# Kernel optimization log

Measured on AMD Instinct MI355X. Metric: run time of the kernel, lower is better.

Reference implementation:

```python
import jax, jax.numpy as jnp
import numpy as np

INPUT_SIZE = 256
HIDDEN_SIZE = 512
BATCH = 128
SEQ_LEN = 512


def setup_inputs() -> dict:
    key = jax.random.key(0)
    ks = jax.random.split(key, 7)
    I, H = INPUT_SIZE, HIDDEN_SIZE
    s_i = 1.0 / np.sqrt(I)
    s_h = 1.0 / np.sqrt(H)
    return {
        "x": jax.random.normal(ks[0], (BATCH, SEQ_LEN, I), dtype=jnp.float32),
        "delta_t": jax.random.uniform(ks[1], (BATCH, SEQ_LEN, 1), dtype=jnp.float32) * 10.0,
        "W": jax.random.normal(ks[2], (I, 4 * H), dtype=jnp.float32) * s_i,
        "U": jax.random.normal(ks[3], (H, 4 * H), dtype=jnp.float32) * s_h,
        "b": jnp.zeros((4 * H,), dtype=jnp.float32),
        "W_d": jax.random.normal(ks[4], (H, H), dtype=jnp.float32) * s_h,
        "b_d": jnp.zeros((H,), dtype=jnp.float32),
    }


def reference(x, delta_t, W, U, b, W_d, b_d):
    # T-LSTM (Baytas et al. 2017): time-decay cell decomposition + standard LSTM gates.
    B, S, _ = x.shape
    H = W_d.shape[0]
    h0 = jnp.zeros((B, H), dtype=x.dtype)
    c0 = jnp.zeros((B, H), dtype=x.dtype)
    E = jnp.float32(np.e)

    def step(carry, inp):
        h, c = carry
        x_t, dt = inp  # (B, I), (B, 1)
        # subspace decomposition with elapsed-time decay g(dt) = 1/log(e + dt)
        c_s = jnp.tanh(c @ W_d + b_d)          # short-term memory
        g = 1.0 / jnp.log(E + dt)              # (B, 1) decay, broadcast over H
        c_adj = c - c_s + c_s * g              # adjusted previous cell state
        z = x_t @ W + h @ U + b                # fused gate pre-activations (B, 4H)
        i_g, f_g, o_g, c_tilde = jnp.split(z, 4, axis=-1)
        i_g = jax.nn.sigmoid(i_g)
        f_g = jax.nn.sigmoid(f_g)
        o_g = jax.nn.sigmoid(o_g)
        c_tilde = jnp.tanh(c_tilde)
        c_new = f_g * c_adj + i_g * c_tilde
        h_new = o_g * jnp.tanh(c_new)
        return (h_new, c_new), h_new

    xs = (jnp.swapaxes(x, 0, 1), jnp.swapaxes(delta_t, 0, 1))  # time-major
    (h_t, c_t), hs = jax.lax.scan(step, (h0, c0), xs)
    outputs = jnp.swapaxes(hs, 0, 1)  # (B, S, H)
    return outputs, h_t, c_t
```

## Files before the change

### kernel.cpp

```cpp
#include <hip/hip_runtime.h>

typedef unsigned short u16;
typedef unsigned int u32;
typedef unsigned long long u64;
typedef __attribute__((ext_vector_type(8))) short short8;
typedef __attribute__((ext_vector_type(4))) float f32x4;

constexpr int BATCH = 128, SEQ = 512, ISZ = 256, HSZ = 512, G4H = 2048;
constexpr int KZ   = ISZ + HSZ;
constexpr int NGRP = 8,  MR  = BATCH / NGRP;
constexpr int NCW  = 32, CPW = HSZ / NCW;
constexpr int LDBZ = KZ + 8, LDBC = HSZ + 8, LDH = HSZ + 8;
constexpr int BH   = BATCH * HSZ;
constexpr size_t BSH = (size_t)BATCH * SEQ * HSZ;

constexpr size_t WUT_OFF = 0;
constexpr size_t WDT_OFF = WUT_OFF + (size_t)G4H * KZ * 2;
constexpr size_t HBF_OFF = WDT_OFF + (size_t)HSZ * HSZ * 2;
constexpr size_t CBF_OFF = HBF_OFF + (size_t)2 * BH * 2;
constexpr size_t FLG_OFF = CBF_OFF + (size_t)2 * BH * 2;

constexpr int BZ_OFF  = 0;
constexpr int BC_OFF  = BZ_OFF  + 64 * LDBZ * 2;
constexpr int HS_OFF  = BC_OFF  + 16 * LDBC * 2;
constexpr int ZS_OFF  = HS_OFF  + MR * LDH * 2;
constexpr int CFL_OFF = ZS_OFF  + 5 * 256 * 4;
constexpr int BL_OFF  = CFL_OFF + MR * CPW * 4;
constexpr int LDS_BYTES = BL_OFF + 5 * CPW * 4;

__device__ __forceinline__ u16 f2bf(float f) {
  unsigned u = __float_as_uint(f);
  u += 0x7fffu + ((u >> 16) & 1u);
  return (u16)(u >> 16);
}

__device__ __forceinline__ u32 cvtpk(float lo, float hi) {
  u32 r;
  asm("v_cvt_pk_bf16_f32 %0, %1, %2" : "=v"(r) : "v"(lo), "v"(hi));
  return r;
}

__device__ __forceinline__ short8 cvt_bf8(float4 a, float4 b) {
  union { u32 u[4]; short8 s; } v;
  v.u[0] = cvtpk(a.x, a.y);
  v.u[1] = cvtpk(a.z, a.w);
  v.u[2] = cvtpk(b.x, b.y);
  v.u[3] = cvtpk(b.z, b.w);
  return v.s;
}

__device__ __forceinline__ u64 ld_at64(const void* p) {
  return __hip_atomic_load((const u64*)p, __ATOMIC_RELAXED,
                           __HIP_MEMORY_SCOPE_AGENT);
}
__device__ __forceinline__ void st_at64(void* p, u64 v) {
  __hip_atomic_store((u64*)p, v, __ATOMIC_RELAXED, __HIP_MEMORY_SCOPE_AGENT);
}
__device__ __forceinline__ void st_at32(void* p, u32 v) {
  __hip_atomic_store((u32*)p, v, __ATOMIC_RELAXED, __HIP_MEMORY_SCOPE_AGENT);
}
__device__ __forceinline__ short8 ld_bf8_at(const u16* p) {
  union { u64 u[2]; short8 s; } v;
  v.u[0] = ld_at64(p);
  v.u[1] = ld_at64(p + 4);
  return v.s;
}

__device__ __forceinline__ float sig_f(float x)  { return 1.f / (1.f + __expf(-x)); }
__device__ __forceinline__ float tanh_f(float x) { return 1.f - 2.f / (1.f + __expf(2.f * x)); }

constexpr int TJ1 = G4H / 32;
constexpr int TK1 = KZ / 32;
constexpr int NT1 = TJ1 * TK1;
constexpr int TJ2 = HSZ / 32;
constexpr int NT2 = TJ2 * TJ2;

__global__ void tlstm_prep(const float* __restrict__ W, const float* __restrict__ U,
                           const float* __restrict__ Wd,
                           u16* __restrict__ wut, u16* __restrict__ wdt,
                           int* __restrict__ flags) {
  __shared__ float tb[32][33];
  const int tid = threadIdx.x;
  const int c = tid & 31, r = tid >> 5;
  const int tile = blockIdx.x;
  if (tile == 0 && tid < 256) flags[tid] = 0;
  if (tile < NT1) {
    const int tj = tile % TJ1, tk = tile / TJ1;
    const int j0 = tj * 32, k0 = tk * 32;
#pragma unroll
    for (int rr = r; rr < 32; rr += 8) {
      const int k = k0 + rr;
      tb[rr][c] = (k < ISZ) ? W[(size_t)k * G4H + j0 + c]
                            : U[(size_t)(k - ISZ) * G4H + j0 + c];
    }
    __syncthreads();
#pragma unroll
    for (int rr = r; rr < 32; rr += 8)
      wut[(size_t)(j0 + rr) * KZ + k0 + c] = f2bf(tb[c][rr]);
  } else {
    const int t2 = tile - NT1;
    const int tj = t2 % TJ2, tk = t2 / TJ2;
    const int j0 = tj * 32, k0 = tk * 32;
#pragma unroll
    for (int rr = r; rr < 32; rr += 8)
      tb[rr][c] = Wd[(size_t)(k0 + rr) * HSZ + j0 + c];
    __syncthreads();
#pragma unroll
    for (int rr = r; rr < 32; rr += 8)
      wdt[(size_t)(j0 + rr) * HSZ + k0 + c] = f2bf(tb[c][rr]);
  }
}

__global__ void __launch_bounds__(320, 1)
tlstm_rec(const float* __restrict__ x, const float* __restrict__ dtp,
          const float* __restrict__ bias, const float* __restrict__ bd,
          const u16* __restrict__ wut, const u16* __restrict__ wdt,
          u16* hbf, u16* cbf, int* flags, float* out) {
  extern __shared__ char lds[];
  u16*   Bz  = (u16*)(lds + BZ_OFF);
  u16*   Bc  = (u16*)(lds + BC_OFF);
  u16*   hs  = (u16*)(lds + HS_OFF);
  float* zs  = (float*)(lds + ZS_OFF);
  float* cfl = (float*)(lds + CFL_OFF);
  float* bl  = (float*)(lds + BL_OFF);

  const int tid  = threadIdx.x;
  const int grp  = blockIdx.x >> 5;
  const int cwg  = blockIdx.x & 31;
  const int G0   = grp * MR;
  const int C0   = cwg * CPW;
  const int wave = tid >> 6, lane = tid & 63;
  const int m16  = lane & 15, quad = lane >> 4;

  {
    const unsigned* src = (const unsigned*)wut;
    unsigned* dst = (unsigned*)Bz;
    for (int i = tid; i < 64 * (KZ / 2); i += 320) {
      int gc = i / (KZ / 2), d = i - gc * (KZ / 2);
      int zc = (gc >> 4) * HSZ + C0 + (gc & 15);
      dst[gc * (LDBZ / 2) + d] = src[zc * (KZ / 2) + d];
    }
    const unsigned* s2 = (const unsigned*)wdt;
    unsigned* d2 = (unsigned*)Bc;
    for (int i = tid; i < 16 * (HSZ / 2); i += 320) {
      int r = i >> 8, d = i & 255;
      d2[r * (LDBC / 2) + d] = s2[(C0 + r) * (HSZ / 2) + d];
    }
  }
  if (tid < 80) {
    int j = tid >> 4, c = tid & 15;
    bl[tid] = (j < 4) ? bias[j * HSZ + C0 + c] : bd[C0 + c];
  }
  if (tid < 256) cfl[tid] = 0.f;
  {
    u64* h0 = (u64*)(hbf + (size_t)G0 * HSZ);
    u64* c0 = (u64*)(cbf + (size_t)G0 * HSZ);
    for (int i = tid; i < MR * HSZ / 4; i += 320) {
      st_at64(h0 + i, 0ull);
      st_at64(c0 + i, 0ull);
    }
  }
  __syncthreads();

  const int* fbase = flags + grp * 32;
  const float* xbase = x + (size_t)(G0 + m16) * SEQ * ISZ + quad * 8;

  for (int t = 0; t < SEQ; ++t) {
    const int p = t & 1, q = p ^ 1;
    const u16* hA = hbf + (size_t)p * BH;
    const u16* cA = cbf + (size_t)p * BH;
    u16* hQ = hbf + (size_t)q * BH;
    u16* cQ = cbf + (size_t)q * BH;

    float dtv = 0.f;
    if (tid < 128)
      dtv = dtp[(size_t)(G0 + (tid >> 3)) * SEQ + t];

    f32x4 acc = {0.f, 0.f, 0.f, 0.f};

    if (wave < 4) {
      const float* xt = xbase + (size_t)t * ISZ;
      float4 xa[16];
#pragma unroll
      for (int kt = 0; kt < 8; ++kt) {
        xa[2 * kt]     = *(const float4*)(xt + kt * 32);
        xa[2 * kt + 1] = *(const float4*)(xt + kt * 32 + 4);
      }
      const u64* src = (const u64*)(hA + (size_t)G0 * HSZ);
      u64 hv[8];
#pragma unroll
      for (int j = 0; j < 8; ++j)
        hv[j] = ld_at64(src + tid + j * 256);

      const u16* bz = Bz + (size_t)(wave * 16 + m16) * LDBZ + quad * 8;
#pragma unroll
      for (int kt = 0; kt < 8; ++kt) {
        short8 a = cvt_bf8(xa[2 * kt], xa[2 * kt + 1]);
        short8 b = *(const short8*)(bz + kt * 32);
        acc = __builtin_amdgcn_mfma_f32_16x16x32_bf16(a, b, acc, 0, 0, 0);
      }
      u64* dst = (u64*)hs;
#pragma unroll
      for (int j = 0; j < 8; ++j) {
        int i = tid + j * 256;
        dst[(i >> 7) * (LDH / 4) + (i & 127)] = hv[j];
      }
    } else {
      const u16* cp = cA + (size_t)(G0 + m16) * HSZ + quad * 8;
      short8 ca[16];
#pragma unroll
      for (int kt = 0; kt < 16; ++kt)
        ca[kt] = ld_bf8_at(cp + kt * 32);
      const u16* bc = Bc + (size_t)m16 * LDBC + quad * 8;
#pragma unroll
      for (int kt = 0; kt < 16; ++kt) {
        short8 b = *(const short8*)(bc + kt * 32);
        acc = __builtin_amdgcn_mfma_f32_16x16x32_bf16(ca[kt], b, acc, 0, 0, 0);
      }
#pragma unroll
      for (int i = 0; i < 4; ++i)
        zs[4 * 256 + (quad * 4 + i) * 16 + m16] = acc[i];
    }
    __syncthreads();

    if (wave < 4) {
      const u16* bz2 = Bz + (size_t)(wave * 16 + m16) * LDBZ + 256 + quad * 8;
      const u16* hp  = hs + (size_t)m16 * LDH + quad * 8;
#pragma unroll
      for (int kt = 0; kt < 16; ++kt) {
        short8 a = *(const short8*)(hp + kt * 32);
        short8 b = *(const short8*)(bz2 + kt * 32);
        acc = __builtin_amdgcn_mfma_f32_16x16x32_bf16(a, b, acc, 0, 0, 0);
      }
#pragma unroll
      for (int i = 0; i < 4; ++i)
        zs[wave * 256 + (quad * 4 + i) * 16 + m16] = acc[i];
    }
    __syncthreads();

    float rh0 = 0.f, rh1 = 0.f, rc0 = 0.f, rc1 = 0.f;
    int row = 0, ch = 0;
    if (tid < 128) {
      const int lr  = tid >> 3;
      const int cp2 = (tid & 7) * 2;
      row = G0 + lr;
      ch  = C0 + cp2;
      const float gdec = 1.f / __logf(2.718281828459045f + dtv);
      float rh[2], rc[2];
#pragma unroll
      for (int u = 0; u < 2; ++u) {
        const int c = cp2 + u;
        const int zb = lr * 16 + c;
        float zi = zs[0 * 256 + zb] + bl[0 * 16 + c];
        float zf = zs[1 * 256 + zb] + bl[1 * 16 + c];
        float zo = zs[2 * 256 + zb] + bl[2 * 16 + c];
        float zc = zs[3 * 256 + zb] + bl[3 * 16 + c];
        float s  = zs[4 * 256 + zb] + bl[4 * 16 + c];
        float cprev = cfl[zb];
        float cs = tanh_f(s);
        float cadj = cprev - cs + cs * gdec;
        float ig = sig_f(zi), fg = sig_f(zf), og = sig_f(zo);
        float ct = tanh_f(zc);
        float cnew = fg * cadj + ig * ct;
        float hnew = og * tanh_f(cnew);
        cfl[zb] = cnew;
        rh[u] = hnew; rc[u] = cnew;
      }
      rh0 = rh[0]; rh1 = rh[1]; rc0 = rc[0]; rc1 = rc[1];
      st_at32(hQ + (size_t)row * HSZ + ch, cvtpk(rh0, rh1));
      st_at32(cQ + (size_t)row * HSZ + ch, cvtpk(rc0, rc1));
    }

    if (t < SEQ - 1) {
      __syncthreads();
      __asm__ volatile("" ::: "memory");
      if (tid == 0)
        __hip_atomic_store(&flags[grp * 32 + cwg], t + 2,
                           __ATOMIC_RELAXED, __HIP_MEMORY_SCOPE_AGENT);
      if (tid < 128) {
        float2 hv2; hv2.x = rh0; hv2.y = rh1;
        *(float2*)(out + ((size_t)row * SEQ + t) * HSZ + ch) = hv2;
      }
      for (;;) {
        int v = (lane < 32)
                    ? __hip_atomic_load(fbase + lane, __ATOMIC_RELAXED,
                                        __HIP_MEMORY_SCOPE_AGENT)
                    : 0x7fffffff;
        if (__all(v >= t + 2)) break;
        __builtin_amdgcn_s_sleep(1);
      }
      __asm__ volatile("" ::: "memory");
    } else {
      if (tid < 128) {
        float2 hv2; hv2.x = rh0; hv2.y = rh1;
        float2 cv2; cv2.x = rc0; cv2.y = rc1;
        *(float2*)(out + ((size_t)row * SEQ + t) * HSZ + ch) = hv2;
        *(float2*)(out + BSH + (size_t)row * HSZ + ch) = hv2;
        *(float2*)(out + BSH + BH + (size_t)row * HSZ + ch) = cv2;
      }
    }
  }
}

extern "C" void kernel_launch(void* const* d_in, const int* in_sizes, int n_in,
                              void* d_out, int out_size, void* d_ws, size_t ws_size,
                              hipStream_t stream) {
  (void)in_sizes; (void)n_in; (void)out_size; (void)ws_size;
  const float* x  = (const float*)d_in[0];
  const float* dt = (const float*)d_in[1];
  const float* W  = (const float*)d_in[2];
  const float* U  = (const float*)d_in[3];
  const float* b  = (const float*)d_in[4];
  const float* Wd = (const float*)d_in[5];
  const float* bd = (const float*)d_in[6];
  float* out = (float*)d_out;
  char*  ws  = (char*)d_ws;

  u16* wut   = (u16*)(ws + WUT_OFF);
  u16* wdt   = (u16*)(ws + WDT_OFF);
  u16* hbf   = (u16*)(ws + HBF_OFF);
  u16* cbf   = (u16*)(ws + CBF_OFF);
  int* flags = (int*)(ws + FLG_OFF);

  tlstm_prep<<<NT1 + NT2, 256, 0, stream>>>(W, U, Wd, wut, wdt, flags);

  hipFuncSetAttribute((const void*)tlstm_rec,
                      hipFuncAttributeMaxDynamicSharedMemorySize, LDS_BYTES);
  tlstm_rec<<<NGRP * NCW, 320, LDS_BYTES, stream>>>(
      x, dt, b, bd, wut, wdt, hbf, cbf, flags, out);
}
```

Before: 3.083 ms.

## Remap batch groups onto XCDs and use XCD-local cache loads for recurrence exchange

At launch each block reads its XCC id, counts blocks per XCD through a control area, and if each of the 8 XCDs holds exactly 32 blocks, reassigns batch groups so that every group sits on a single XCD. In that mode the h/c state and flag exchanges use plain loads with the sc0 bit and plain stores, which are meant to stay within the shared per-XCD L2 instead of agent-scope atomics. The next step's x tile and dt are prefetched and converted to bf16 while waiting on flags, which takes the input fetch off the critical path. The change adds a cooperative launch, a fallback path, and a bounded spin that breaks after a fixed count, and correctness relies on the coherence assumptions about XCD-local L2.

New measurement: 4.988 ms. 1.62x slower.

```diff
diff --git a/kernel.cpp b/kernel.cpp
--- a/kernel.cpp
+++ b/kernel.cpp
@@ -5,6 +5,7 @@
 typedef unsigned long long u64;
 typedef __attribute__((ext_vector_type(8))) short short8;
 typedef __attribute__((ext_vector_type(4))) float f32x4;
+typedef __attribute__((ext_vector_type(4))) unsigned int u32x4;
 
 constexpr int BATCH = 128, SEQ = 512, ISZ = 256, HSZ = 512, G4H = 2048;
 constexpr int KZ   = ISZ + HSZ;
@@ -28,6 +29,7 @@
 constexpr int BL_OFF  = CFL_OFF + MR * CPW * 4;
 constexpr int LDS_BYTES = BL_OFF + 5 * CPW * 4;
 
+
 __device__ __forceinline__ u16 f2bf(float f) {
   unsigned u = __float_as_uint(f);
   u += 0x7fffu + ((u >> 16) & 1u);
@@ -59,15 +61,74 @@
 __device__ __forceinline__ void st_at32(void* p, u32 v) {
   __hip_atomic_store((u32*)p, v, __ATOMIC_RELAXED, __HIP_MEMORY_SCOPE_AGENT);
 }
-__device__ __forceinline__ short8 ld_bf8_at(const u16* p) {
-  union { u64 u[2]; short8 s; } v;
-  v.u[0] = ld_at64(p);
-  v.u[1] = ld_at64(p + 4);
-  return v.s;
+__device__ __forceinline__ int ld_ati(const int* p) {
+  return __hip_atomic_load(p, __ATOMIC_RELAXED, __HIP_MEMORY_SCOPE_AGENT);
+}
+
+template<bool LOCAL>
+__device__ __forceinline__ u64 ld64g(const u64* p) {
+  if constexpr (LOCAL) {
+    u64 r;
+    asm volatile("global_load_dwordx2 %0, %1, off sc0" : "=v"(r) : "v"(p));
+    return r;
+  } else {
+    return ld_at64(p);
+  }
+}
+
+template<bool LOCAL>
+__device__ __forceinline__ short8 ld128g(const u16* p) {
+  if constexpr (LOCAL) {
+    union { u32x4 u; short8 s; } r;
+    asm volatile("global_load_dwordx4 %0, %1, off sc0" : "=v"(r.u) : "v"(p));
+    return r.s;
+  } else {
+    union { u64 u[2]; short8 s; } v;
+    v.u[0] = ld_at64(p);
+    v.u[1] = ld_at64(p + 4);
+    return v.s;
+  }
+}
+
+template<bool LOCAL>
+__device__ __forceinline__ void wait_vm0() {
+  if constexpr (LOCAL) {
+    asm volatile("s_waitcnt vmcnt(0)" ::: "memory");
+    __builtin_amdgcn_sched_barrier(0);
+  }
+}
+
+template<bool LOCAL>
+__device__ __forceinline__ int ldflag(const int* p) {
+  if constexpr (LOCAL) {
+    int r;
+    asm volatile("global_load_dword %0, %1, off sc0\n\ts_waitcnt vmcnt(0)"
+                 : "=v"(r) : "v"(p) : "memory");
+    return r;
+  } else {
+    return ld_ati(p);
+  }
+}
+
+template<bool LOCAL>
+__device__ __forceinline__ void stflag(int* p, int v) {
+  if constexpr (LOCAL) {
+    asm volatile("global_store_dword %0, %1, off" :: "v"(p), "v"(v) : "memory");
+  } else {
+    __hip_atomic_store(p, v, __ATOMIC_RELAXED, __HIP_MEMORY_SCOPE_AGENT);
+  }
 }
 
 __device__ __forceinline__ float sig_f(float x)  { return 1.f / (1.f + __expf(-x)); }
 __device__ __forceinline__ float tanh_f(float x) { return 1.f - 2.f / (1.f + __expf(2.f * x)); }
+
+__device__ __forceinline__ int spin_ctl(int* p, int target) {
+  for (int i = 0; i < (1 << 18); ++i) {
+    if (ld_ati(p) >= target) return 1;
+    __builtin_amdgcn_s_sleep(8);
+  }
+  return 0;
+}
 
 constexpr int TJ1 = G4H / 32;
 constexpr int TK1 = KZ / 32;
@@ -83,7 +144,12 @@
   const int tid = threadIdx.x;
   const int c = tid & 31, r = tid >> 5;
   const int tile = blockIdx.x;
+  int* ctl = flags + 256;
   if (tile == 0 && tid < 256) flags[tid] = 0;
+  if ((tile == 1 || tile == 2) && tid < 256) {
+    int i = (tile - 1) * 256 + tid;
+    ctl[i] = (i == 10) ? 1 : 0;
+  }
   if (tile < NT1) {
     const int tj = tile % TJ1, tk = tile / TJ1;
     const int j0 = tj * 32, k0 = tk * 32;
@@ -111,12 +177,11 @@
   }
 }
 
-__global__ void __launch_bounds__(320, 1)
-tlstm_rec(const float* __restrict__ x, const float* __restrict__ dtp,
-          const float* __restrict__ bias, const float* __restrict__ bd,
-          const u16* __restrict__ wut, const u16* __restrict__ wdt,
-          u16* hbf, u16* cbf, int* flags, float* out) {
-  extern __shared__ char lds[];
+template<bool LOCAL>
+__device__ __forceinline__ void run_loop(
+    const float* __restrict__ x, const float* __restrict__ dtp,
+    u16* hbf, u16* cbf, int* flags, float* out,
+    char* lds, const int tid, const int grp, const int cwg) {
   u16*   Bz  = (u16*)(lds + BZ_OFF);
   u16*   Bc  = (u16*)(lds + BC_OFF);
   u16*   hs  = (u16*)(lds + HS_OFF);
@@ -124,46 +189,28 @@
   float* cfl = (float*)(lds + CFL_OFF);
   float* bl  = (float*)(lds + BL_OFF);
 
-  const int tid  = threadIdx.x;
-  const int grp  = blockIdx.x >> 5;
-  const int cwg  = blockIdx.x & 31;
   const int G0   = grp * MR;
   const int C0   = cwg * CPW;
   const int wave = tid >> 6, lane = tid & 63;
   const int m16  = lane & 15, quad = lane >> 4;
-
-  {
-    const unsigned* src = (const unsigned*)wut;
-    unsigned* dst = (unsigned*)Bz;
-    for (int i = tid; i < 64 * (KZ / 2); i += 320) {
-      int gc = i / (KZ / 2), d = i - gc * (KZ / 2);
-      int zc = (gc >> 4) * HSZ + C0 + (gc & 15);
-      dst[gc * (LDBZ / 2) + d] = src[zc * (KZ / 2) + d];
-    }
-    const unsigned* s2 = (const unsigned*)wdt;
-    unsigned* d2 = (unsigned*)Bc;
-    for (int i = tid; i < 16 * (HSZ / 2); i += 320) {
-      int r = i >> 8, d = i & 255;
-      d2[r * (LDBC / 2) + d] = s2[(C0 + r) * (HSZ / 2) + d];
-    }
-  }
-  if (tid < 80) {
-    int j = tid >> 4, c = tid & 15;
-    bl[tid] = (j < 4) ? bias[j * HSZ + C0 + c] : bd[C0 + c];
-  }
-  if (tid < 256) cfl[tid] = 0.f;
-  {
-    u64* h0 = (u64*)(hbf + (size_t)G0 * HSZ);
-    u64* c0 = (u64*)(cbf + (size_t)G0 * HSZ);
-    for (int i = tid; i < MR * HSZ / 4; i += 320) {
-      st_at64(h0 + i, 0ull);
-      st_at64(c0 + i, 0ull);
-    }
-  }
-  __syncthreads();
-
   const int* fbase = flags + grp * 32;
   const float* xbase = x + (size_t)(G0 + m16) * SEQ * ISZ + quad * 8;
+  const int drow = G0 + (tid >> 3);
+
+  short8 xa8[8];
+  float dtn = 0.f;
+  if (wave < 4) {
+    float4 xf[16];
+#pragma unroll
+    for (int kt = 0; kt < 8; ++kt) {
+      xf[2 * kt]     = *(const float4*)(xbase + kt * 32);
+      xf[2 * kt + 1] = *(const float4*)(xbase + kt * 32 + 4);
+    }
+#pragma unroll
+    for (int kt = 0; kt < 8; ++kt)
+      xa8[kt] = cvt_bf8(xf[2 * kt], xf[2 * kt + 1]);
+  }
+  if (tid < 128) dtn = dtp[(size_t)drow * SEQ];
 
   for (int t = 0; t < SEQ; ++t) {
     const int p = t & 1, q = p ^ 1;
@@ -171,34 +218,24 @@
     const u16* cA = cbf + (size_t)p * BH;
     u16* hQ = hbf + (size_t)q * BH;
     u16* cQ = cbf + (size_t)q * BH;
-
-    float dtv = 0.f;
-    if (tid < 128)
-      dtv = dtp[(size_t)(G0 + (tid >> 3)) * SEQ + t];
+    const float dtv = dtn;
 
     f32x4 acc = {0.f, 0.f, 0.f, 0.f};
 
     if (wave < 4) {
-      const float* xt = xbase + (size_t)t * ISZ;
-      float4 xa[16];
-#pragma unroll
-      for (int kt = 0; kt < 8; ++kt) {
-        xa[2 * kt]     = *(const float4*)(xt + kt * 32);
-        xa[2 * kt + 1] = *(const float4*)(xt + kt * 32 + 4);
-      }
       const u64* src = (const u64*)(hA + (size_t)G0 * HSZ);
       u64 hv[8];
 #pragma unroll
       for (int j = 0; j < 8; ++j)
-        hv[j] = ld_at64(src + tid + j * 256);
+        hv[j] = ld64g<LOCAL>(src + tid + j * 256);
 
       const u16* bz = Bz + (size_t)(wave * 16 + m16) * LDBZ + quad * 8;
 #pragma unroll
       for (int kt = 0; kt < 8; ++kt) {
-        short8 a = cvt_bf8(xa[2 * kt], xa[2 * kt + 1]);
         short8 b = *(const short8*)(bz + kt * 32);
-        acc = __builtin_amdgcn_mfma_f32_16x16x32_bf16(a, b, acc, 0, 0, 0);
-      }
+        acc = __builtin_amdgcn_mfma_f32_16x16x32_bf16(xa8[kt], b, acc, 0, 0, 0);
+      }
+      wait_vm0<LOCAL>();
       u64* dst = (u64*)hs;
 #pragma unroll
       for (int j = 0; j < 8; ++j) {
@@ -210,7 +247,8 @@
       short8 ca[16];
 #pragma unroll
       for (int kt = 0; kt < 16; ++kt)
-        ca[kt] = ld_bf8_at(cp + kt * 32);
+        ca[kt] = ld128g<LOCAL>(cp + kt * 32);
+      wait_vm0<LOCAL>();
       const u16* bc = Bc + (size_t)m16 * LDBC + quad * 8;
 #pragma unroll
       for (int kt = 0; kt < 16; ++kt) {
@@ -267,26 +305,42 @@
         rh[u] = hnew; rc[u] = cnew;
       }
       rh0 = rh[0]; rh1 = rh[1]; rc0 = rc[0]; rc1 = rc[1];
-      st_at32(hQ + (size_t)row * HSZ + ch, cvtpk(rh0, rh1));
-      st_at32(cQ + (size_t)row * HSZ + ch, cvtpk(rc0, rc1));
+      if constexpr (LOCAL) {
+        *(u32*)(hQ + (size_t)row * HSZ + ch) = cvtpk(rh0, rh1);
+        *(u32*)(cQ + (size_t)row * HSZ + ch) = cvtpk(rc0, rc1);
+      } else {
+        st_at32(hQ + (size_t)row * HSZ + ch, cvtpk(rh0, rh1));
+        st_at32(cQ + (size_t)row * HSZ + ch, cvtpk(rc0, rc1));
+      }
     }
 
     if (t < SEQ - 1) {
       __syncthreads();
       __asm__ volatile("" ::: "memory");
       if (tid == 0)
-        __hip_atomic_store(&flags[grp * 32 + cwg], t + 2,
-                           __ATOMIC_RELAXED, __HIP_MEMORY_SCOPE_AGENT);
+        stflag<LOCAL>(&flags[grp * 32 + cwg], t + 2);
       if (tid < 128) {
         float2 hv2; hv2.x = rh0; hv2.y = rh1;
         *(float2*)(out + ((size_t)row * SEQ + t) * HSZ + ch) = hv2;
       }
-      for (;;) {
-        int v = (lane < 32)
-                    ? __hip_atomic_load(fbase + lane, __ATOMIC_RELAXED,
-                                        __HIP_MEMORY_SCOPE_AGENT)
-                    : 0x7fffffff;
+      if (wave < 4) {
+        const float* xn = xbase + (size_t)(t + 1) * ISZ;
+        float4 xf[16];
+#pragma unroll
+        for (int kt = 0; kt < 8; ++kt) {
+          xf[2 * kt]     = *(const float4*)(xn + kt * 32);
+          xf[2 * kt + 1] = *(const float4*)(xn + kt * 32 + 4);
+        }
+#pragma unroll
+        for (int kt = 0; kt < 8; ++kt)
+          xa8[kt] = cvt_bf8(xf[2 * kt], xf[2 * kt + 1]);
+      }
+      if (tid < 128)
+        dtn = dtp[(size_t)drow * SEQ + t + 1];
+      for (int gu = 0; ; ++gu) {
+        int v = (lane < 32) ? ldflag<LOCAL>(fbase + lane) : 0x7fffffff;
         if (__all(v >= t + 2)) break;
+        if (gu > (1 << 22)) break;
         __builtin_amdgcn_s_sleep(1);
       }
       __asm__ volatile("" ::: "memory");
@@ -300,6 +354,109 @@
       }
     }
   }
+}
+
+__global__ void __launch_bounds__(320, 1)
+tlstm_rec(const float* __restrict__ x, const float* __restrict__ dtp,
+          const float* __restrict__ bias, const float* __restrict__ bd,
+          const u16* __restrict__ wut, const u16* __restrict__ wdt,
+          u16* hbf, u16* cbf, int* flags, float* out, int allow_local) {
+  extern __shared__ char lds[];
+  __shared__ int sh[3];
+  const int tid = threadIdx.x;
+  int* ctl = flags + 256;
+
+  if (tid == 0) {
+    int g = blockIdx.x >> 5, c = blockIdx.x & 31, mode = 0;
+    if (allow_local) {
+      u32 xcc;
+      asm volatile("s_getreg_b32 %0, hwreg(20, 0, 32)" : "=s"(xcc));
+      const int myx = (int)(xcc & 7u);
+      const int slot = __hip_atomic_fetch_add(&ctl[myx], 1, __ATOMIC_RELAXED,
+                                              __HIP_MEMORY_SCOPE_AGENT);
+      __hip_atomic_fetch_add(&ctl[8], 1, __ATOMIC_RELAXED,
+                             __HIP_MEMORY_SCOPE_AGENT);
+      int ok1 = spin_ctl(&ctl[8], 256);
+      bool bal = (ok1 != 0);
+      if (bal)
+        for (int i = 0; i < 8; ++i)
+          bal &= (ld_ati(&ctl[i]) == 32);
+      if (bal && slot < 32) {
+        int* tw = &ctl[64 + myx * 32 + slot];
+        int mg = 0x5A130000 | (myx << 8) | slot;
+        asm volatile("global_store_dword %0, %1, off\n\ts_waitcnt vmcnt(0)"
+                     :: "v"(tw), "v"(mg) : "memory");
+      } else {
+        __hip_atomic_fetch_and(&ctl[10], 0, __ATOMIC_RELAXED,
+                               __HIP_MEMORY_SCOPE_AGENT);
+      }
+      __hip_atomic_fetch_add(&ctl[9], 1, __ATOMIC_RELAXED,
+                             __HIP_MEMORY_SCOPE_AGENT);
+      if (!spin_ctl(&ctl[9], 256)) bal = false;
+      if (bal) {
+        int ok = 1;
+        for (int i = 0; i < 32; ++i) {
+          int tv;
+          const int* tp = &ctl[64 + myx * 32 + i];
+          asm volatile("global_load_dword %0, %1, off sc0\n\ts_waitcnt vmcnt(0)"
+                       : "=v"(tv) : "v"(tp) : "memory");
+          ok &= (tv == (0x5A130000 | (myx << 8) | i));
+        }
+        if (!ok)
+          __hip_atomic_fetch_and(&ctl[10], 0, __ATOMIC_RELAXED,
+                                 __HIP_MEMORY_SCOPE_AGENT);
+      }
+      __hip_atomic_fetch_add(&ctl[12], 1, __ATOMIC_RELAXED,
+                             __HIP_MEMORY_SCOPE_AGENT);
+      if (!spin_ctl(&ctl[12], 256)) bal = false;
+      mode = bal ? ld_ati(&ctl[10]) : 0;
+      if (mode) { g = myx; c = slot; }
+    }
+    sh[0] = g; sh[1] = c; sh[2] = mode;
+  }
+  __syncthreads();
+  const int grp = sh[0], cwg = sh[1], mode = sh[2];
+  const int G0 = grp * MR, C0 = cwg * CPW;
+
+  u16*   Bz  = (u16*)(lds + BZ_OFF);
+  u16*   Bc  = (u16*)(lds + BC_OFF);
+  float* cfl = (float*)(lds + CFL_OFF);
+  float* bl  = (float*)(lds + BL_OFF);
+
+  {
+    const unsigned* src = (const unsigned*)wut;
+    unsigned* dst = (unsigned*)Bz;
+    for (int i = tid; i < 64 * (KZ / 2); i += 320) {
+      int gc = i / (KZ / 2), d = i - gc * (KZ / 2);
+      int zc = (gc >> 4) * HSZ + C0 + (gc & 15);
+      dst[gc * (LDBZ / 2) + d] = src[zc * (KZ / 2) + d];
+    }
+    const unsigned* s2 = (const unsigned*)wdt;
+    unsigned* d2 = (unsigned*)Bc;
+    for (int i = tid; i < 16 * (HSZ / 2); i += 320) {
+      int r = i >> 8, d = i & 255;
+      d2[r * (LDBC / 2) + d] = s2[(C0 + r) * (HSZ / 2) + d];
+    }
+  }
+  if (tid < 80) {
+    int j = tid >> 4, c = tid & 15;
+    bl[tid] = (j < 4) ? bias[j * HSZ + C0 + c] : bd[C0 + c];
+  }
+  if (tid < 256) cfl[tid] = 0.f;
+  {
+    u64* h0 = (u64*)(hbf + (size_t)G0 * HSZ);
+    u64* c0 = (u64*)(cbf + (size_t)G0 * HSZ);
+    for (int i = tid; i < MR * HSZ / 4; i += 320) {
+      st_at64(h0 + i, 0ull);
+      st_at64(c0 + i, 0ull);
+    }
+  }
+  __syncthreads();
+
+  if (mode)
+    run_loop<true>(x, dtp, hbf, cbf, flags, out, lds, tid, grp, cwg);
+  else
+    run_loop<false>(x, dtp, hbf, cbf, flags, out, lds, tid, grp, cwg);
 }
 
 extern "C" void kernel_launch(void* const* d_in, const int* in_sizes, int n_in,
@@ -326,6 +483,17 @@
 
   hipFuncSetAttribute((const void*)tlstm_rec,
                       hipFuncAttributeMaxDynamicSharedMemorySize, LDS_BYTES);
-  tlstm_rec<<<NGRP * NCW, 320, LDS_BYTES, stream>>>(
-      x, dt, b, bd, wut, wdt, hbf, cbf, flags, out);
-}
+
+  int allow = 1;
+  void* args[11] = {(void*)&x, (void*)&dt, (void*)&b, (void*)&bd,
+                    (void*)&wut, (void*)&wdt, (void*)&hbf, (void*)&cbf,
+                    (void*)&flags, (void*)&out, (void*)&allow};
+  hipError_t e = hipLaunchCooperativeKernel((const void*)tlstm_rec,
+                                            dim3(NGRP * NCW), dim3(320),
+                                            args, LDS_BYTES, stream);
+  if (e != hipSuccess) {
+    (void)hipGetLastError();
+    tlstm_rec<<<NGRP * NCW, 320, LDS_BYTES, stream>>>(
+        x, dt, b, bd, wut, wdt, hbf, cbf, flags, out, 0);
+  }
+}
```

## Interleave two batch groups per workgroup to overlap recurrence latency

Applied to the files above, without the earlier changes.

Each workgroup now processes two batch groups (A and B), halving the grid to 128 blocks. The gate computation for B is interleaved with A's cell update, and A's flag is published before B's work so other blocks can proceed sooner. Cell state moves to registers, the next step's x and dt are prefetched and converted to bf16 ahead of time, and the flag wait moves to the start of the step with a bounded spin. The aim is to hide cross-block synchronisation and global-load latency at the cost of more per-block work, fewer active CUs, and more registers.

After: 4.642 ms. 1.51x slower.

```diff
diff --git a/kernel.cpp b/kernel.cpp
--- a/kernel.cpp
+++ b/kernel.cpp
@@ -10,6 +10,7 @@
 constexpr int KZ   = ISZ + HSZ;
 constexpr int NGRP = 8,  MR  = BATCH / NGRP;
 constexpr int NCW  = 32, CPW = HSZ / NCW;
+constexpr int NPAIR = 4;
 constexpr int LDBZ = KZ + 8, LDBC = HSZ + 8, LDH = HSZ + 8;
 constexpr int BH   = BATCH * HSZ;
 constexpr size_t BSH = (size_t)BATCH * SEQ * HSZ;
@@ -22,10 +23,11 @@
 
 constexpr int BZ_OFF  = 0;
 constexpr int BC_OFF  = BZ_OFF  + 64 * LDBZ * 2;
-constexpr int HS_OFF  = BC_OFF  + 16 * LDBC * 2;
-constexpr int ZS_OFF  = HS_OFF  + MR * LDH * 2;
-constexpr int CFL_OFF = ZS_OFF  + 5 * 256 * 4;
-constexpr int BL_OFF  = CFL_OFF + MR * CPW * 4;
+constexpr int HSA_OFF = BC_OFF  + 16 * LDBC * 2;
+constexpr int HSB_OFF = HSA_OFF + MR * LDH * 2;
+constexpr int ZSA_OFF = HSB_OFF + MR * LDH * 2;
+constexpr int ZSB_OFF = ZSA_OFF + 5 * 256 * 4;
+constexpr int BL_OFF  = ZSB_OFF + 5 * 256 * 4;
 constexpr int LDS_BYTES = BL_OFF + 5 * CPW * 4;
 
 __device__ __forceinline__ u16 f2bf(float f) {
@@ -59,6 +61,9 @@
 __device__ __forceinline__ void st_at32(void* p, u32 v) {
   __hip_atomic_store((u32*)p, v, __ATOMIC_RELAXED, __HIP_MEMORY_SCOPE_AGENT);
 }
+__device__ __forceinline__ int ld_ati(const int* p) {
+  return __hip_atomic_load(p, __ATOMIC_RELAXED, __HIP_MEMORY_SCOPE_AGENT);
+}
 __device__ __forceinline__ short8 ld_bf8_at(const u16* p) {
   union { u64 u[2]; short8 s; } v;
   v.u[0] = ld_at64(p);
@@ -68,6 +73,49 @@
 
 __device__ __forceinline__ float sig_f(float x)  { return 1.f / (1.f + __expf(-x)); }
 __device__ __forceinline__ float tanh_f(float x) { return 1.f - 2.f / (1.f + __expf(2.f * x)); }
+
+__device__ __forceinline__ void barl() {
+  asm volatile("s_waitcnt lgkmcnt(0)" ::: "memory");
+  __builtin_amdgcn_s_barrier();
+  __builtin_amdgcn_sched_barrier(0);
+}
+
+__device__ __forceinline__ void xfetch(const float* xp, short8* xa8) {
+  float4 xf[16];
+#pragma unroll
+  for (int kt = 0; kt < 8; ++kt) {
+    xf[2 * kt]     = *(const float4*)(xp + kt * 32);
+    xf[2 * kt + 1] = *(const float4*)(xp + kt * 32 + 4);
+  }
+#pragma unroll
+  for (int kt = 0; kt < 8; ++kt)
+    xa8[kt] = cvt_bf8(xf[2 * kt], xf[2 * kt + 1]);
+}
+
+__device__ __forceinline__ void tcell(const float* zsg, const float* bl,
+    float dtv, int lr, int cp2, float& cprev0, float& cprev1,
+    float& rh0, float& rh1, float& rc0, float& rc1) {
+  const float gdec = 1.f / __logf(2.718281828459045f + dtv);
+#pragma unroll
+  for (int u = 0; u < 2; ++u) {
+    const int c = cp2 + u;
+    const int zb = lr * 16 + c;
+    float zi = zsg[0 * 256 + zb] + bl[0 * 16 + c];
+    float zf = zsg[1 * 256 + zb] + bl[1 * 16 + c];
+    float zo = zsg[2 * 256 + zb] + bl[2 * 16 + c];
+    float zc = zsg[3 * 256 + zb] + bl[3 * 16 + c];
+    float s  = zsg[4 * 256 + zb] + bl[4 * 16 + c];
+    float cprev = u ? cprev1 : cprev0;
+    float cs = tanh_f(s);
+    float cadj = cprev - cs + cs * gdec;
+    float ig = sig_f(zi), fg = sig_f(zf), og = sig_f(zo);
+    float ct = tanh_f(zc);
+    float cnew = fg * cadj + ig * ct;
+    float hnew = og * tanh_f(cnew);
+    if (u) { cprev1 = cnew; rh1 = hnew; rc1 = cnew; }
+    else   { cprev0 = cnew; rh0 = hnew; rc0 = cnew; }
+  }
+}
 
 constexpr int TJ1 = G4H / 32;
 constexpr int TK1 = KZ / 32;
@@ -119,15 +167,17 @@
   extern __shared__ char lds[];
   u16*   Bz  = (u16*)(lds + BZ_OFF);
   u16*   Bc  = (u16*)(lds + BC_OFF);
-  u16*   hs  = (u16*)(lds + HS_OFF);
-  float* zs  = (float*)(lds + ZS_OFF);
-  float* cfl = (float*)(lds + CFL_OFF);
+  u16*   hsA = (u16*)(lds + HSA_OFF);
+  u16*   hsB = (u16*)(lds + HSB_OFF);
+  float* zsA = (float*)(lds + ZSA_OFF);
+  float* zsB = (float*)(lds + ZSB_OFF);
   float* bl  = (float*)(lds + BL_OFF);
 
   const int tid  = threadIdx.x;
-  const int grp  = blockIdx.x >> 5;
+  const int pid  = blockIdx.x >> 5;
   const int cwg  = blockIdx.x & 31;
-  const int G0   = grp * MR;
+  const int gA   = pid, gB = pid + NPAIR;
+  const int G0a  = gA * MR, G0b = gB * MR;
   const int C0   = cwg * CPW;
   const int wave = tid >> 6, lane = tid & 63;
   const int m16  = lane & 15, quad = lane >> 4;
@@ -151,66 +201,81 @@
     int j = tid >> 4, c = tid & 15;
     bl[tid] = (j < 4) ? bias[j * HSZ + C0 + c] : bd[C0 + c];
   }
-  if (tid < 256) cfl[tid] = 0.f;
   {
-    u64* h0 = (u64*)(hbf + (size_t)G0 * HSZ);
-    u64* c0 = (u64*)(cbf + (size_t)G0 * HSZ);
+    u64* h0a = (u64*)(hbf + (size_t)G0a * HSZ);
+    u64* c0a = (u64*)(cbf + (size_t)G0a * HSZ);
+    u64* h0b = (u64*)(hbf + (size_t)G0b * HSZ);
+    u64* c0b = (u64*)(cbf + (size_t)G0b * HSZ);
     for (int i = tid; i < MR * HSZ / 4; i += 320) {
-      st_at64(h0 + i, 0ull);
-      st_at64(c0 + i, 0ull);
+      st_at64(h0a + i, 0ull); st_at64(c0a + i, 0ull);
+      st_at64(h0b + i, 0ull); st_at64(c0b + i, 0ull);
     }
   }
   __syncthreads();
 
-  const int* fbase = flags + grp * 32;
-  const float* xbase = x + (size_t)(G0 + m16) * SEQ * ISZ + quad * 8;
+  const float* xbA = x + (size_t)(G0a + m16) * SEQ * ISZ + quad * 8;
+  const float* xbB = x + (size_t)(G0b + m16) * SEQ * ISZ + quad * 8;
+  const int drA = G0a + (tid >> 3), drB = G0b + (tid >> 3);
+
+  short8 xa8a[8], xa8b[8];
+  float dtnA = 0.f, dtnB = 0.f;
+  if (wave < 4) { xfetch(xbA, xa8a); xfetch(xbB, xa8b); }
+  if (tid < 128) { dtnA = dtp[(size_t)drA * SEQ]; dtnB = dtp[(size_t)drB * SEQ]; }
+  float cpa0 = 0.f, cpa1 = 0.f, cpb0 = 0.f, cpb1 = 0.f;
 
   for (int t = 0; t < SEQ; ++t) {
     const int p = t & 1, q = p ^ 1;
-    const u16* hA = hbf + (size_t)p * BH;
-    const u16* cA = cbf + (size_t)p * BH;
+    const u16* hP = hbf + (size_t)p * BH;
+    const u16* cP = cbf + (size_t)p * BH;
     u16* hQ = hbf + (size_t)q * BH;
     u16* cQ = cbf + (size_t)q * BH;
-
-    float dtv = 0.f;
-    if (tid < 128)
-      dtv = dtp[(size_t)(G0 + (tid >> 3)) * SEQ + t];
-
-    f32x4 acc = {0.f, 0.f, 0.f, 0.f};
+    const float dtvA = dtnA, dtvB = dtnB;
+
+    if (t > 0) {
+      for (int gu = 0; ; ++gu) {
+        int v = (lane < 32) ? ld_ati(flags + gA * 32 + lane)
+                            : ld_ati(flags + gB * 32 + (lane - 32));
+        if (__all(v >= t)) break;
+        if (gu > (1 << 22)) break;
+        __builtin_amdgcn_s_sleep(1);
+      }
+      __asm__ volatile("" ::: "memory");
+    }
+
+    f32x4 acc  = {0.f, 0.f, 0.f, 0.f};
+    f32x4 accB = {0.f, 0.f, 0.f, 0.f};
+    short8 cb[16];
 
     if (wave < 4) {
-      const float* xt = xbase + (size_t)t * ISZ;
-      float4 xa[16];
+      const u64* sA = (const u64*)(hP + (size_t)G0a * HSZ);
+      const u64* sB = (const u64*)(hP + (size_t)G0b * HSZ);
+      u64 ha[8], hb[8];
+#pragma unroll
+      for (int j = 0; j < 8; ++j) ha[j] = ld_at64(sA + tid + j * 256);
+#pragma unroll
+      for (int j = 0; j < 8; ++j) hb[j] = ld_at64(sB + tid + j * 256);
+      const u16* bz = Bz + (size_t)(wave * 16 + m16) * LDBZ + quad * 8;
 #pragma unroll
       for (int kt = 0; kt < 8; ++kt) {
-        xa[2 * kt]     = *(const float4*)(xt + kt * 32);
-        xa[2 * kt + 1] = *(const float4*)(xt + kt * 32 + 4);
-      }
-      const u64* src = (const u64*)(hA + (size_t)G0 * HSZ);
-      u64 hv[8];
-#pragma unroll
-      for (int j = 0; j < 8; ++j)
-        hv[j] = ld_at64(src + tid + j * 256);
-
-      const u16* bz = Bz + (size_t)(wave * 16 + m16) * LDBZ + quad * 8;
-#pragma unroll
-      for (int kt = 0; kt < 8; ++kt) {
-        short8 a = cvt_bf8(xa[2 * kt], xa[2 * kt + 1]);
         short8 b = *(const short8*)(bz + kt * 32);
-        acc = __builtin_amdgcn_mfma_f32_16x16x32_bf16(a, b, acc, 0, 0, 0);
-      }
-      u64* dst = (u64*)hs;
+        acc = __builtin_amdgcn_mfma_f32_16x16x32_bf16(xa8a[kt], b, acc, 0, 0, 0);
+      }
+      u64* dA = (u64*)hsA; u64* dB = (u64*)hsB;
 #pragma unroll
       for (int j = 0; j < 8; ++j) {
         int i = tid + j * 256;
-        dst[(i >> 7) * (LDH / 4) + (i & 127)] = hv[j];
+        dA[(i >> 7) * (LDH / 4) + (i & 127)] = ha[j];
+      }
+#pragma unroll
+      for (int j = 0; j < 8; ++j) {
+        int i = tid + j * 256;
+        dB[(i >> 7) * (LDH / 4) + (i & 127)] = hb[j];
       }
     } else {
-      const u16* cp = cA + (size_t)(G0 + m16) * HSZ + quad * 8;
+      const u16* cpA = cP + (size_t)(G0a + m16) * HSZ + quad * 8;
       short8 ca[16];
 #pragma unroll
-      for (int kt = 0; kt < 16; ++kt)
-        ca[kt] = ld_bf8_at(cp + kt * 32);
+      for (int kt = 0; kt < 16; ++kt) ca[kt] = ld_bf8_at(cpA + kt * 32);
       const u16* bc = Bc + (size_t)m16 * LDBC + quad * 8;
 #pragma unroll
       for (int kt = 0; kt < 16; ++kt) {
@@ -219,13 +284,16 @@
       }
 #pragma unroll
       for (int i = 0; i < 4; ++i)
-        zs[4 * 256 + (quad * 4 + i) * 16 + m16] = acc[i];
-    }
-    __syncthreads();
+        zsA[4 * 256 + (quad * 4 + i) * 16 + m16] = acc[i];
+      const u16* cpB = cP + (size_t)(G0b + m16) * HSZ + quad * 8;
+#pragma unroll
+      for (int kt = 0; kt < 16; ++kt) cb[kt] = ld_bf8_at(cpB + kt * 32);
+    }
+    barl();
 
     if (wave < 4) {
       const u16* bz2 = Bz + (size_t)(wave * 16 + m16) * LDBZ + 256 + quad * 8;
-      const u16* hp  = hs + (size_t)m16 * LDH + quad * 8;
+      const u16* hp  = hsA + (size_t)m16 * LDH + quad * 8;
 #pragma unroll
       for (int kt = 0; kt < 16; ++kt) {
         short8 a = *(const short8*)(hp + kt * 32);
@@ -234,69 +302,94 @@
       }
 #pragma unroll
       for (int i = 0; i < 4; ++i)
-        zs[wave * 256 + (quad * 4 + i) * 16 + m16] = acc[i];
+        zsA[wave * 256 + (quad * 4 + i) * 16 + m16] = acc[i];
+    } else {
+      const u16* bc = Bc + (size_t)m16 * LDBC + quad * 8;
+#pragma unroll
+      for (int kt = 0; kt < 16; ++kt) {
+        short8 b = *(const short8*)(bc + kt * 32);
+        accB = __builtin_amdgcn_mfma_f32_16x16x32_bf16(cb[kt], b, accB, 0, 0, 0);
+      }
+#pragma unroll
+      for (int i = 0; i < 4; ++i)
+        zsB[4 * 256 + (quad * 4 + i) * 16 + m16] = accB[i];
+    }
+    barl();
+
+    float rha0 = 0.f, rha1 = 0.f, rca0 = 0.f, rca1 = 0.f;
+    int rowA = 0, chA = 0;
+    if (tid < 128) {
+      const int lr = tid >> 3, cp2 = (tid & 7) * 2;
+      rowA = G0a + lr; chA = C0 + cp2;
+      tcell(zsA, bl, dtvA, lr, cp2, cpa0, cpa1, rha0, rha1, rca0, rca1);
+      st_at32(hQ + (size_t)rowA * HSZ + chA, cvtpk(rha0, rha1));
+      st_at32(cQ + (size_t)rowA * HSZ + chA, cvtpk(rca0, rca1));
+    }
+
+    if (wave < 4) {
+      const u16* bz = Bz + (size_t)(wave * 16 + m16) * LDBZ + quad * 8;
+#pragma unroll
+      for (int kt = 0; kt < 8; ++kt) {
+        short8 b = *(const short8*)(bz + kt * 32);
+        accB = __builtin_amdgcn_mfma_f32_16x16x32_bf16(xa8b[kt], b, accB, 0, 0, 0);
+      }
+      const u16* bz2 = bz + 256;
+      const u16* hp  = hsB + (size_t)m16 * LDH + quad * 8;
+#pragma unroll
+      for (int kt = 0; kt < 16; ++kt) {
+        short8 a = *(const short8*)(hp + kt * 32);
+        short8 b = *(const short8*)(bz2 + kt * 32);
+        accB = __builtin_amdgcn_mfma_f32_16x16x32_bf16(a, b, accB, 0, 0, 0);
+      }
+#pragma unroll
+      for (int i = 0; i < 4; ++i)
+        zsB[wave * 256 + (quad * 4 + i) * 16 + m16] = accB[i];
     }
     __syncthreads();
-
-    float rh0 = 0.f, rh1 = 0.f, rc0 = 0.f, rc1 = 0.f;
-    int row = 0, ch = 0;
+    if (t < SEQ - 1 && tid == 0)
+      st_at32((u32*)&flags[gA * 32 + cwg], (u32)(t + 1));
     if (tid < 128) {
-      const int lr  = tid >> 3;
-      const int cp2 = (tid & 7) * 2;
-      row = G0 + lr;
-      ch  = C0 + cp2;
-      const float gdec = 1.f / __logf(2.718281828459045f + dtv);
-      float rh[2], rc[2];
-#pragma unroll
-      for (int u = 0; u < 2; ++u) {
-        const int c = cp2 + u;
-        const int zb = lr * 16 + c;
-        float zi = zs[0 * 256 + zb] + bl[0 * 16 + c];
-        float zf = zs[1 * 256 + zb] + bl[1 * 16 + c];
-        float zo = zs[2 * 256 + zb] + bl[2 * 16 + c];
-        float zc = zs[3 * 256 + zb] + bl[3 * 16 + c];
-        float s  = zs[4 * 256 + zb] + bl[4 * 16 + c];
-        float cprev = cfl[zb];
-        float cs = tanh_f(s);
-        float cadj = cprev - cs + cs * gdec;
-        float ig = sig_f(zi), fg = sig_f(zf), og = sig_f(zo);
-        float ct = tanh_f(zc);
-        float cnew = fg * cadj + ig * ct;
-        float hnew = og * tanh_f(cnew);
-        cfl[zb] = cnew;
-        rh[u] = hnew; rc[u] = cnew;
-      }
-      rh0 = rh[0]; rh1 = rh[1]; rc0 = rc[0]; rc1 = rc[1];
-      st_at32(hQ + (size_t)row * HSZ + ch, cvtpk(rh0, rh1));
-      st_at32(cQ + (size_t)row * HSZ + ch, cvtpk(rc0, rc1));
-    }
-
+      float2 hv2; hv2.x = rha0; hv2.y = rha1;
+      *(float2*)(out + ((size_t)rowA * SEQ + t) * HSZ + chA) = hv2;
+      if (t == SEQ - 1) {
+        float2 cv2; cv2.x = rca0; cv2.y = rca1;
+        *(float2*)(out + BSH + (size_t)rowA * HSZ + chA) = hv2;
+        *(float2*)(out + BSH + BH + (size_t)rowA * HSZ + chA) = cv2;
+      }
+    }
+
+    float rhb0 = 0.f, rhb1 = 0.f, rcb0 = 0.f, rcb1 = 0.f;
+    int rowB = 0, chB = 0;
+    if (tid < 128) {
+      const int lr = tid >> 3, cp2 = (tid & 7) * 2;
+      rowB = G0b + lr; chB = C0 + cp2;
+      tcell(zsB, bl, dtvB, lr, cp2, cpb0, cpb1, rhb0, rhb1, rcb0, rcb1);
+      st_at32(hQ + (size_t)rowB * HSZ + chB, cvtpk(rhb0, rhb1));
+      st_at32(cQ + (size_t)rowB * HSZ + chB, cvtpk(rcb0, rcb1));
+    }
+    __syncthreads();
     if (t < SEQ - 1) {
-      __syncthreads();
-      __asm__ volatile("" ::: "memory");
       if (tid == 0)
-        __hip_atomic_store(&flags[grp * 32 + cwg], t + 2,
-                           __ATOMIC_RELAXED, __HIP_MEMORY_SCOPE_AGENT);
+        st_at32((u32*)&flags[gB * 32 + cwg], (u32)(t + 1));
       if (tid < 128) {
-        float2 hv2; hv2.x = rh0; hv2.y = rh1;
-        *(float2*)(out + ((size_t)row * SEQ + t) * HSZ + ch) = hv2;
-      }
-      for (;;) {
-        int v = (lane < 32)
-                    ? __hip_atomic_load(fbase + lane, __ATOMIC_RELAXED,
-                                        __HIP_MEMORY_SCOPE_AGENT)
-                    : 0x7fffffff;
-        if (__all(v >= t + 2)) break;
-        __builtin_amdgcn_s_sleep(1);
-      }
-      __asm__ volatile("" ::: "memory");
+        float2 hv2; hv2.x = rhb0; hv2.y = rhb1;
+        *(float2*)(out + ((size_t)rowB * SEQ + t) * HSZ + chB) = hv2;
+      }
+      if (wave < 4) {
+        xfetch(xbA + (size_t)(t + 1) * ISZ, xa8a);
+        xfetch(xbB + (size_t)(t + 1) * ISZ, xa8b);
+      }
+      if (tid < 128) {
+        dtnA = dtp[(size_t)drA * SEQ + t + 1];
+        dtnB = dtp[(size_t)drB * SEQ + t + 1];
+      }
     } else {
       if (tid < 128) {
-        float2 hv2; hv2.x = rh0; hv2.y = rh1;
-        float2 cv2; cv2.x = rc0; cv2.y = rc1;
-        *(float2*)(out + ((size_t)row * SEQ + t) * HSZ + ch) = hv2;
-        *(float2*)(out + BSH + (size_t)row * HSZ + ch) = hv2;
-        *(float2*)(out + BSH + BH + (size_t)row * HSZ + ch) = cv2;
+        float2 hv2; hv2.x = rhb0; hv2.y = rhb1;
+        float2 cv2; cv2.x = rcb0; cv2.y = rcb1;
+        *(float2*)(out + ((size_t)rowB * SEQ + t) * HSZ + chB) = hv2;
+        *(float2*)(out + BSH + (size_t)rowB * HSZ + chB) = hv2;
+        *(float2*)(out + BSH + BH + (size_t)rowB * HSZ + chB) = cv2;
       }
     }
   }
@@ -326,6 +419,6 @@
 
   hipFuncSetAttribute((const void*)tlstm_rec,
                       hipFuncAttributeMaxDynamicSharedMemorySize, LDS_BYTES);
-  tlstm_rec<<<NGRP * NCW, 320, LDS_BYTES, stream>>>(
+  tlstm_rec<<<NPAIR * NCW, 320, LDS_BYTES, stream>>>(
       x, dt, b, bd, wut, wdt, hbf, cbf, flags, out);
 }
```

## Prefetch next-step x/dt during spin wait and fuse h GEMM into one phase

Applied to the files above, without the earlier changes.

The gate waves now load h straight from global memory into registers and run the x and h MFMAs back-to-back. This removes the LDS staging of h and one block barrier per step. The x and delta_t loads for step t+1, including the bf16 conversion, are issued before the inter-block flag spin, so their latency overlaps the wait. The cell state is kept in registers instead of LDS, the remaining barrier is a lighter lgkmcnt-wait barrier, and the spin loop gains an iteration cap that could silently break synchronisation if it is ever hit.

Measured after the change: 4.068 ms. 1.32x slower.

```diff
diff --git a/kernel.cpp b/kernel.cpp
--- a/kernel.cpp
+++ b/kernel.cpp
@@ -10,7 +10,7 @@
 constexpr int KZ   = ISZ + HSZ;
 constexpr int NGRP = 8,  MR  = BATCH / NGRP;
 constexpr int NCW  = 32, CPW = HSZ / NCW;
-constexpr int LDBZ = KZ + 8, LDBC = HSZ + 8, LDH = HSZ + 8;
+constexpr int LDBZ = KZ + 8, LDBC = HSZ + 8;
 constexpr int BH   = BATCH * HSZ;
 constexpr size_t BSH = (size_t)BATCH * SEQ * HSZ;
 
@@ -22,10 +22,8 @@
 
 constexpr int BZ_OFF  = 0;
 constexpr int BC_OFF  = BZ_OFF  + 64 * LDBZ * 2;
-constexpr int HS_OFF  = BC_OFF  + 16 * LDBC * 2;
-constexpr int ZS_OFF  = HS_OFF  + MR * LDH * 2;
-constexpr int CFL_OFF = ZS_OFF  + 5 * 256 * 4;
-constexpr int BL_OFF  = CFL_OFF + MR * CPW * 4;
+constexpr int ZS_OFF  = BC_OFF  + 16 * LDBC * 2;
+constexpr int BL_OFF  = ZS_OFF  + 5 * 256 * 4;
 constexpr int LDS_BYTES = BL_OFF + 5 * CPW * 4;
 
 __device__ __forceinline__ u16 f2bf(float f) {
@@ -59,6 +57,9 @@
 __device__ __forceinline__ void st_at32(void* p, u32 v) {
   __hip_atomic_store((u32*)p, v, __ATOMIC_RELAXED, __HIP_MEMORY_SCOPE_AGENT);
 }
+__device__ __forceinline__ int ld_ati(const int* p) {
+  return __hip_atomic_load(p, __ATOMIC_RELAXED, __HIP_MEMORY_SCOPE_AGENT);
+}
 __device__ __forceinline__ short8 ld_bf8_at(const u16* p) {
   union { u64 u[2]; short8 s; } v;
   v.u[0] = ld_at64(p);
@@ -68,6 +69,24 @@
 
 __device__ __forceinline__ float sig_f(float x)  { return 1.f / (1.f + __expf(-x)); }
 __device__ __forceinline__ float tanh_f(float x) { return 1.f - 2.f / (1.f + __expf(2.f * x)); }
+
+__device__ __forceinline__ void barl() {
+  asm volatile("s_waitcnt lgkmcnt(0)" ::: "memory");
+  __builtin_amdgcn_s_barrier();
+  __builtin_amdgcn_sched_barrier(0);
+}
+
+__device__ __forceinline__ void xfetch(const float* xp, short8* xa8) {
+  float4 xf[16];
+#pragma unroll
+  for (int kt = 0; kt < 8; ++kt) {
+    xf[2 * kt]     = *(const float4*)(xp + kt * 32);
+    xf[2 * kt + 1] = *(const float4*)(xp + kt * 32 + 4);
+  }
+#pragma unroll
+  for (int kt = 0; kt < 8; ++kt)
+    xa8[kt] = cvt_bf8(xf[2 * kt], xf[2 * kt + 1]);
+}
 
 constexpr int TJ1 = G4H / 32;
 constexpr int TK1 = KZ / 32;
@@ -119,9 +138,7 @@
   extern __shared__ char lds[];
   u16*   Bz  = (u16*)(lds + BZ_OFF);
   u16*   Bc  = (u16*)(lds + BC_OFF);
-  u16*   hs  = (u16*)(lds + HS_OFF);
   float* zs  = (float*)(lds + ZS_OFF);
-  float* cfl = (float*)(lds + CFL_OFF);
   float* bl  = (float*)(lds + BL_OFF);
 
   const int tid  = threadIdx.x;
@@ -151,7 +168,6 @@
     int j = tid >> 4, c = tid & 15;
     bl[tid] = (j < 4) ? bias[j * HSZ + C0 + c] : bd[C0 + c];
   }
-  if (tid < 256) cfl[tid] = 0.f;
   {
     u64* h0 = (u64*)(hbf + (size_t)G0 * HSZ);
     u64* c0 = (u64*)(cbf + (size_t)G0 * HSZ);
@@ -164,6 +180,13 @@
 
   const int* fbase = flags + grp * 32;
   const float* xbase = x + (size_t)(G0 + m16) * SEQ * ISZ + quad * 8;
+  const int drow = G0 + (tid >> 3);
+
+  short8 xa8[8];
+  float dtn = 0.f;
+  if (wave < 4) xfetch(xbase, xa8);
+  if (tid < 128) dtn = dtp[(size_t)drow * SEQ];
+  float cm0 = 0.f, cm1 = 0.f;
 
   for (int t = 0; t < SEQ; ++t) {
     const int p = t & 1, q = p ^ 1;
@@ -171,40 +194,31 @@
     const u16* cA = cbf + (size_t)p * BH;
     u16* hQ = hbf + (size_t)q * BH;
     u16* cQ = cbf + (size_t)q * BH;
-
-    float dtv = 0.f;
-    if (tid < 128)
-      dtv = dtp[(size_t)(G0 + (tid >> 3)) * SEQ + t];
+    const float dtv = dtn;
 
     f32x4 acc = {0.f, 0.f, 0.f, 0.f};
 
     if (wave < 4) {
-      const float* xt = xbase + (size_t)t * ISZ;
-      float4 xa[16];
+      const u16* hp = hA + (size_t)(G0 + m16) * HSZ + quad * 8;
+      short8 hf[16];
+#pragma unroll
+      for (int kt = 0; kt < 16; ++kt)
+        hf[kt] = ld_bf8_at(hp + kt * 32);
+      const u16* bz = Bz + (size_t)(wave * 16 + m16) * LDBZ + quad * 8;
 #pragma unroll
       for (int kt = 0; kt < 8; ++kt) {
-        xa[2 * kt]     = *(const float4*)(xt + kt * 32);
-        xa[2 * kt + 1] = *(const float4*)(xt + kt * 32 + 4);
-      }
-      const u64* src = (const u64*)(hA + (size_t)G0 * HSZ);
-      u64 hv[8];
-#pragma unroll
-      for (int j = 0; j < 8; ++j)
-        hv[j] = ld_at64(src + tid + j * 256);
-
-      const u16* bz = Bz + (size_t)(wave * 16 + m16) * LDBZ + quad * 8;
-#pragma unroll
-      for (int kt = 0; kt < 8; ++kt) {
-        short8 a = cvt_bf8(xa[2 * kt], xa[2 * kt + 1]);
         short8 b = *(const short8*)(bz + kt * 32);
-        acc = __builtin_amdgcn_mfma_f32_16x16x32_bf16(a, b, acc, 0, 0, 0);
-      }
-      u64* dst = (u64*)hs;
-#pragma unroll
-      for (int j = 0; j < 8; ++j) {
-        int i = tid + j * 256;
-        dst[(i >> 7) * (LDH / 4) + (i & 127)] = hv[j];
-      }
+        acc = __builtin_amdgcn_mfma_f32_16x16x32_bf16(xa8[kt], b, acc, 0, 0, 0);
+      }
+      const u16* bz2 = bz + 256;
+#pragma unroll
+      for (int kt = 0; kt < 16; ++kt) {
+        short8 b = *(const short8*)(bz2 + kt * 32);
+        acc = __builtin_amdgcn_mfma_f32_16x16x32_bf16(hf[kt], b, acc, 0, 0, 0);
+      }
+#pragma unroll
+      for (int i = 0; i < 4; ++i)
+        zs[wave * 256 + (quad * 4 + i) * 16 + m16] = acc[i];
     } else {
       const u16* cp = cA + (size_t)(G0 + m16) * HSZ + quad * 8;
       short8 ca[16];
@@ -221,22 +235,7 @@
       for (int i = 0; i < 4; ++i)
         zs[4 * 256 + (quad * 4 + i) * 16 + m16] = acc[i];
     }
-    __syncthreads();
-
-    if (wave < 4) {
-      const u16* bz2 = Bz + (size_t)(wave * 16 + m16) * LDBZ + 256 + quad * 8;
-      const u16* hp  = hs + (size_t)m16 * LDH + quad * 8;
-#pragma unroll
-      for (int kt = 0; kt < 16; ++kt) {
-        short8 a = *(const short8*)(hp + kt * 32);
-        short8 b = *(const short8*)(bz2 + kt * 32);
-        acc = __builtin_amdgcn_mfma_f32_16x16x32_bf16(a, b, acc, 0, 0, 0);
-      }
-#pragma unroll
-      for (int i = 0; i < 4; ++i)
-        zs[wave * 256 + (quad * 4 + i) * 16 + m16] = acc[i];
-    }
-    __syncthreads();
+    barl();
 
     float rh0 = 0.f, rh1 = 0.f, rc0 = 0.f, rc1 = 0.f;
     int row = 0, ch = 0;
@@ -256,17 +255,16 @@
         float zo = zs[2 * 256 + zb] + bl[2 * 16 + c];
         float zc = zs[3 * 256 + zb] + bl[3 * 16 + c];
         float s  = zs[4 * 256 + zb] + bl[4 * 16 + c];
-        float cprev = cfl[zb];
+        float cprev = u ? cm1 : cm0;
         float cs = tanh_f(s);
         float cadj = cprev - cs + cs * gdec;
         float ig = sig_f(zi), fg = sig_f(zf), og = sig_f(zo);
         float ct = tanh_f(zc);
         float cnew = fg * cadj + ig * ct;
         float hnew = og * tanh_f(cnew);
-        cfl[zb] = cnew;
-        rh[u] = hnew; rc[u] = cnew;
-      }
-      rh0 = rh[0]; rh1 = rh[1]; rc0 = rc[0]; rc1 = rc[1];
+        if (u) { cm1 = cnew; rh1 = hnew; rc1 = cnew; }
+        else   { cm0 = cnew; rh0 = hnew; rc0 = cnew; }
+      }
       st_at32(hQ + (size_t)row * HSZ + ch, cvtpk(rh0, rh1));
       st_at32(cQ + (size_t)row * HSZ + ch, cvtpk(rc0, rc1));
     }
@@ -275,18 +273,19 @@
       __syncthreads();
       __asm__ volatile("" ::: "memory");
       if (tid == 0)
-        __hip_atomic_store(&flags[grp * 32 + cwg], t + 2,
-                           __ATOMIC_RELAXED, __HIP_MEMORY_SCOPE_AGENT);
+        st_at32((u32*)&flags[grp * 32 + cwg], (u32)(t + 2));
       if (tid < 128) {
         float2 hv2; hv2.x = rh0; hv2.y = rh1;
         *(float2*)(out + ((size_t)row * SEQ + t) * HSZ + ch) = hv2;
       }
-      for (;;) {
-        int v = (lane < 32)
-                    ? __hip_atomic_load(fbase + lane, __ATOMIC_RELAXED,
-                                        __HIP_MEMORY_SCOPE_AGENT)
-                    : 0x7fffffff;
+      if (wave < 4)
+        xfetch(xbase + (size_t)(t + 1) * ISZ, xa8);
+      if (tid < 128)
+        dtn = dtp[(size_t)drow * SEQ + t + 1];
+      for (int gu = 0; ; ++gu) {
+        int v = (lane < 32) ? ld_ati(fbase + lane) : 0x7fffffff;
         if (__all(v >= t + 2)) break;
+        if (gu > (1 << 22)) break;
         __builtin_amdgcn_s_sleep(1);
       }
       __asm__ volatile("" ::: "memory");
```
